# Optimization experiments

Hardware: AMD Instinct MI355X
Metric: run time of the kernel (lower is better)

The kernel has to match this reference:

```python
import jax, jax.numpy as jnp
import numpy as np

B, L, HID = 1, 2048, 4096
H, KV, D = 32, 2, 128
ROT = int(D * 0.5)  # partial rotary dims per head
THETA = 10000.0
SCALE = D ** -0.5


def _rope_tables(L, rot, theta):
    inv_freq = 1.0 / (theta ** (np.arange(0, rot, 2, dtype=np.float32) / rot))  # [rot/2]
    t = np.arange(L, dtype=np.float32)
    freqs = np.outer(t, inv_freq)  # [L, rot/2]
    return jnp.asarray(np.cos(freqs)), jnp.asarray(np.sin(freqs))


def setup_inputs() -> dict:
    key = jax.random.key(0)
    ks = jax.random.split(key, 8)
    s = HID ** -0.5
    x = jax.random.normal(ks[0], (B, L, HID), dtype=jnp.float32)
    Wq = jax.random.normal(ks[1], (HID, H * D), dtype=jnp.float32) * s
    Wk = jax.random.normal(ks[2], (HID, KV * D), dtype=jnp.float32) * s
    Wv = jax.random.normal(ks[3], (HID, KV * D), dtype=jnp.float32) * s
    Wo = jax.random.normal(ks[4], (H * D, HID), dtype=jnp.float32) * s
    bq = jax.random.normal(ks[5], (H * D,), dtype=jnp.float32) * 0.01
    bk = jax.random.normal(ks[6], (KV * D,), dtype=jnp.float32) * 0.01
    bv = jax.random.normal(ks[7], (KV * D,), dtype=jnp.float32) * 0.01
    cos, sin = _rope_tables(L, ROT, THETA)
    # additive causal mask
    causal = jnp.tril(jnp.ones((L, L), dtype=bool))
    attention_mask = jnp.where(causal, 0.0, -1e9)[None, None].astype(jnp.float32)
    return {"x": x, "Wq": Wq, "bq": bq, "Wk": Wk, "bk": bk, "Wv": Wv, "bv": bv,
            "Wo": Wo, "cos": cos, "sin": sin, "attention_mask": attention_mask}


def _apply_rope(t, cos, sin):
    # t: [B, h, L, D]; rotary on first ROT dims, pass-through on the rest
    t_rot, t_pass = t[..., :ROT], t[..., ROT:]
    x1, x2 = t_rot[..., : ROT // 2], t_rot[..., ROT // 2:]
    c = cos[None, None]  # [1,1,L,ROT/2]
    s = sin[None, None]
    rot = jnp.concatenate([x1 * c - x2 * s, x2 * c + x1 * s], axis=-1)
    return jnp.concatenate([rot, t_pass], axis=-1)


def reference(x, Wq, bq, Wk, bk, Wv, bv, Wo, cos, sin, attention_mask):
    Bx, Lx, _ = x.shape
    q = (x @ Wq + bq).reshape(Bx, Lx, H, D).transpose(0, 2, 1, 3)   # [B,H,L,D]
    k = (x @ Wk + bk).reshape(Bx, Lx, KV, D).transpose(0, 2, 1, 3)  # [B,KV,L,D]
    v = (x @ Wv + bv).reshape(Bx, Lx, KV, D).transpose(0, 2, 1, 3)
    q = _apply_rope(q, cos, sin)
    k = _apply_rope(k, cos, sin)
    # GQA: repeat KV heads
    rep = H // KV
    k = jnp.repeat(k, rep, axis=1)  # [B,H,L,D]
    v = jnp.repeat(v, rep, axis=1)
    w = jnp.einsum('bhqd,bhkd->bhqk', q, k) * SCALE + attention_mask
    w = jax.nn.softmax(w, axis=-1)
    o = jnp.einsum('bhqk,bhkd->bhqd', w, v)
    o = o.transpose(0, 2, 1, 3).reshape(Bx, Lx, H * D)
    return o @ Wo
```

## Files before the change

kernel.cpp:

```cpp
#include <hip/hip_runtime.h>
#include <stdint.h>

#define L_SEQ 2048
#define HID   4096
#define NH    32
#define NKV   2
#define DH    128
#define NQKV  4608
#define QSCALE 0.088388347648318447f

typedef __bf16 bf16x8 __attribute__((ext_vector_type(8)));
typedef float  f32x4  __attribute__((ext_vector_type(4)));

__device__ __forceinline__ unsigned short f2bf(float f) {
  union { float f; unsigned u; } cv; cv.f = f;
  unsigned u = cv.u;
  return (unsigned short)((u + 0x7fffu + ((u >> 16) & 1u)) >> 16);
}
__device__ __forceinline__ float bf2f(unsigned short h) {
  union { unsigned u; float f; } cv; cv.u = (unsigned)h << 16; return cv.f;
}

#define GLL16(gsrc, ldst)                                                              \
  __builtin_amdgcn_global_load_lds(                                                    \
      (const __attribute__((address_space(1))) unsigned int*)(gsrc),                   \
      (__attribute__((address_space(3))) unsigned int*)(ldst), 16, 0, 0)

__global__ __launch_bounds__(256) void cast_bf16_kernel(const float* __restrict__ in,
                                                        unsigned short* __restrict__ out,
                                                        int n4) {
  int i = blockIdx.x * 256 + threadIdx.x;
  if (i >= n4) return;
  float4 v = reinterpret_cast<const float4*>(in)[i];
  ushort4 o;
  o.x = f2bf(v.x); o.y = f2bf(v.y); o.z = f2bf(v.z); o.w = f2bf(v.w);
  reinterpret_cast<ushort4*>(out)[i] = o;
}

__global__ __launch_bounds__(256) void transpose_cast_kernel(const float* __restrict__ in,
                                                             unsigned short* __restrict__ out,
                                                             int R, int C) {
  __shared__ float tile[64][65];
  const int c0 = blockIdx.x * 64, r0 = blockIdx.y * 64;
  const int tid = threadIdx.x;
  #pragma unroll
  for (int it = 0; it < 4; ++it) {
    int row = it * 16 + (tid >> 4);
    float4 v = *reinterpret_cast<const float4*>(&in[(size_t)(r0 + row) * C + c0 + (tid & 15) * 4]);
    tile[row][(tid & 15) * 4 + 0] = v.x;
    tile[row][(tid & 15) * 4 + 1] = v.y;
    tile[row][(tid & 15) * 4 + 2] = v.z;
    tile[row][(tid & 15) * 4 + 3] = v.w;
  }
  __syncthreads();
  #pragma unroll
  for (int it = 0; it < 8; ++it) {
    int c  = it * 8 + (tid >> 5);
    int rp = tid & 31;
    unsigned u = (unsigned)f2bf(tile[2 * rp][c]) | ((unsigned)f2bf(tile[2 * rp + 1][c]) << 16);
    *reinterpret_cast<unsigned*>(&out[(size_t)(c0 + c) * R + r0 + 2 * rp]) = u;
  }
}

__global__ __launch_bounds__(256) void vtrans_kernel(const unsigned short* __restrict__ in,
                                                     unsigned short* __restrict__ out) {
  __shared__ unsigned short tile[64][72];
  const int l0 = blockIdx.x * 64, d0 = blockIdx.y * 64, g = blockIdx.z;
  const int tid = threadIdx.x;
  #pragma unroll
  for (int it = 0; it < 2; ++it) {
    int l = it * 32 + (tid >> 3);
    *reinterpret_cast<uint4*>(&tile[l][(tid & 7) * 8]) =
        *reinterpret_cast<const uint4*>(&in[((size_t)g * L_SEQ + l0 + l) * DH + d0 + (tid & 7) * 8]);
  }
  __syncthreads();
  #pragma unroll
  for (int it = 0; it < 2; ++it) {
    int d = it * 32 + (tid >> 3);
    unsigned short tmp[8];
    #pragma unroll
    for (int e = 0; e < 8; ++e) tmp[e] = tile[(tid & 7) * 8 + e][d];
    *reinterpret_cast<uint4*>(&out[((size_t)g * DH + d0 + d) * L_SEQ + l0 + (tid & 7) * 8]) =
        *reinterpret_cast<uint4*>(tmp);
  }
}

#define TBM 128
#define TBN 128
#define TBK 64

template <int MODE>
__global__ __launch_bounds__(256, 2) void gemm128_kernel(const unsigned short* __restrict__ A,
                                                         const unsigned short* __restrict__ Bt,
                                                         float* __restrict__ C,
                                                         const float* __restrict__ bq,
                                                         const float* __restrict__ bk,
                                                         const float* __restrict__ bv,
                                                         const float* __restrict__ cosT,
                                                         const float* __restrict__ sinT,
                                                         unsigned short* __restrict__ qb,
                                                         unsigned short* __restrict__ kb,
                                                         unsigned short* __restrict__ vlin,
                                                         int M, int N, int K) {
  __shared__ __attribute__((aligned(16))) unsigned short As[2][TBM * TBK];
  __shared__ __attribute__((aligned(16))) unsigned short Bs[2][TBN * TBK];
  const int tid = threadIdx.x;
  const int wave = tid >> 6, lane = tid & 63;
  const int lg = lane >> 4, ll = lane & 15;
  const int wm = wave >> 1, wn = wave & 1;

  int gx = gridDim.x, nwg = gx * gridDim.y;
  int flat = blockIdx.y * gx + blockIdx.x;
  int bx = blockIdx.x, by = blockIdx.y;
  if ((nwg & 7) == 0) {
    int t = (flat & 7) * (nwg >> 3) + (flat >> 3);
    bx = t % gx; by = t / gx;
  }
  const int m0 = by * TBM, n0 = bx * TBN;

  f32x4 acc[4][4] = {};
  const int NT = K >> 6;

  auto stage = [&](int t, int buf) {
    const int k0 = t * TBK;
    #pragma unroll
    for (int i = 0; i < 4; ++i) {
      int ci  = (i * 4 + wave) * 64 + lane;
      int row = ci >> 3;
      int cg  = (ci & 7) ^ (row & 7);
      GLL16(A + (size_t)(m0 + row) * K + k0 + cg * 8, &As[buf][(i * 4 + wave) * 512]);
    }
    #pragma unroll
    for (int i = 0; i < 4; ++i) {
      int ci  = (i * 4 + wave) * 64 + lane;
      int row = ci >> 3;
      int cg  = (ci & 7) ^ (row & 7);
      GLL16(Bt + (size_t)(n0 + row) * K + k0 + cg * 8, &Bs[buf][(i * 4 + wave) * 512]);
    }
  };

  stage(0, 0);
  stage(1, 1);

  for (int t = 0; t < NT; ++t) {
    const int cur = t & 1;
    if (t + 1 < NT) asm volatile("s_waitcnt vmcnt(8)" ::: "memory");
    else            asm volatile("s_waitcnt vmcnt(0)" ::: "memory");
    __builtin_amdgcn_s_barrier();

    const unsigned short* Ac = &As[cur][0];
    const unsigned short* Bc = &Bs[cur][0];
    bf16x8 afr[2][4], bfr[2][4];
    #pragma unroll
    for (int kk = 0; kk < 2; ++kk)
      #pragma unroll
      for (int i = 0; i < 4; ++i) {
        int ra = wm * 64 + i * 16 + ll;
        afr[kk][i] = *reinterpret_cast<const bf16x8*>(
            &Ac[ra * 64 + (((kk * 4 + lg) ^ (ra & 7)) * 8)]);
        int rb = wn * 64 + i * 16 + ll;
        bfr[kk][i] = *reinterpret_cast<const bf16x8*>(
            &Bc[rb * 64 + (((kk * 4 + lg) ^ (rb & 7)) * 8)]);
      }
    asm volatile("s_waitcnt lgkmcnt(0)" ::: "memory");
    __builtin_amdgcn_s_barrier();
    if (t + 2 < NT) stage(t + 2, cur);

    __builtin_amdgcn_s_setprio(1);
    #pragma unroll
    for (int kk = 0; kk < 2; ++kk)
      #pragma unroll
      for (int i = 0; i < 4; ++i)
        #pragma unroll
        for (int j = 0; j < 4; ++j)
          acc[i][j] = __builtin_amdgcn_mfma_f32_16x16x32_bf16(afr[kk][i], bfr[kk][j],
                                                              acc[i][j], 0, 0, 0);
    __builtin_amdgcn_s_setprio(0);
  }

  if (MODE == 0) {
    #pragma unroll
    for (int i = 0; i < 4; ++i)
      #pragma unroll
      for (int j = 0; j < 4; ++j) {
        int col  = n0 + wn * 64 + j * 16 + ll;
        int rowb = m0 + wm * 64 + i * 16 + lg * 4;
        #pragma unroll
        for (int r = 0; r < 4; ++r)
          C[(size_t)(rowb + r) * N + col] = acc[i][j][r];
      }
  } else {
    const int region = (n0 < 4096) ? 0 : ((n0 < 4352) ? 1 : 2);
    const int hh = (region == 0) ? (n0 >> 7) : ((region == 1) ? ((n0 - 4096) >> 7) : ((n0 - 4352) >> 7));
    const float* bias = (region == 0) ? bq : ((region == 1) ? bk : bv);
    #pragma unroll
    for (int j = 0; j < 4; ++j) {
      float bj = bias[hh * DH + wn * 64 + j * 16 + ll];
      #pragma unroll
      for (int i = 0; i < 4; ++i)
        #pragma unroll
        for (int r = 0; r < 4; ++r) acc[i][j][r] += bj;
    }
    if (region < 2 && wn == 0) {
      #pragma unroll
      for (int i = 0; i < 4; ++i)
        #pragma unroll
        for (int r = 0; r < 4; ++r) {
          int l = m0 + wm * 64 + i * 16 + lg * 4 + r;
          float c0 = cosT[l * 32 + ll],      s0 = sinT[l * 32 + ll];
          float c1 = cosT[l * 32 + 16 + ll], s1 = sinT[l * 32 + 16 + ll];
          float x10 = acc[i][0][r], x20 = acc[i][2][r];
          float x11 = acc[i][1][r], x21 = acc[i][3][r];
          acc[i][0][r] = x10 * c0 - x20 * s0;
          acc[i][2][r] = x20 * c0 + x10 * s0;
          acc[i][1][r] = x11 * c1 - x21 * s1;
          acc[i][3][r] = x21 * c1 + x11 * s1;
        }
    }
    const float scale = (region == 0) ? QSCALE : 1.f;
    unsigned short* dst = (region == 0) ? qb : ((region == 1) ? kb : vlin);
    #pragma unroll
    for (int i = 0; i < 4; ++i)
      #pragma unroll
      for (int j = 0; j < 4; ++j) {
        int d = wn * 64 + j * 16 + ll;
        #pragma unroll
        for (int r = 0; r < 4; ++r) {
          int l = m0 + wm * 64 + i * 16 + lg * 4 + r;
          dst[((size_t)hh * L_SEQ + l) * DH + d] = f2bf(acc[i][j][r] * scale);
        }
      }
  }
}

__global__ __launch_bounds__(256) void attn_kernel(const unsigned short* __restrict__ qg,
                                                   const unsigned short* __restrict__ kb,
                                                   const unsigned short* __restrict__ vt,
                                                   unsigned short* __restrict__ ob) {
  __shared__ __attribute__((aligned(16))) unsigned short Ks[2][64 * 128];
  __shared__ __attribute__((aligned(16))) unsigned short Vs[2][128 * 64];
  __shared__ __attribute__((aligned(16))) unsigned short Ps[4][16 * 64];

  const int pair = blockIdx.x, h = blockIdx.y;
  const int g = h >> 4;
  const int tid = threadIdx.x, wave = tid >> 6, lane = tid & 63;
  const int lg = lane >> 4, ll = lane & 15;

  const int krow = (lane >> 4);
  const int kcg0 = (lane & 15);
  const int vrow = (lane >> 3);
  const int vcg0 = (lane & 7);

  #pragma unroll
  for (int seg = 0; seg < 2; ++seg) {
    const int qt = seg ? (31 - pair) : pair;
    const int q0 = qt * 64 + wave * 16;

    bf16x8 qf[4];
    #pragma unroll
    for (int f = 0; f < 4; ++f)
      qf[f] = *reinterpret_cast<const bf16x8*>(
          qg + ((size_t)h * L_SEQ + q0 + ll) * DH + f * 32 + lg * 8);

    f32x4 of[8] = {};
    float m = -1e30f, lsum = 0.f;

    const int kvN = qt + 1;
    int cur = 0;

    #pragma unroll
    for (int c = 0; c < 4; ++c) {
      int issue = wave * 4 + c;
      int rk = issue * 4 + krow;
      GLL16(kb + ((size_t)g * L_SEQ + rk) * DH + (kcg0 ^ (rk & 7)) * 8, &Ks[0][issue * 512]);
      int rv = issue * 8 + vrow;
      GLL16(vt + ((size_t)g * DH + rv) * L_SEQ + (vcg0 ^ (rv & 7)) * 8, &Vs[0][issue * 512]);
    }
    __syncthreads();

    for (int t = 0; t < kvN; ++t) {
      if (t + 1 < kvN) {
        int kv1 = (t + 1) * 64;
        #pragma unroll
        for (int c = 0; c < 4; ++c) {
          int issue = wave * 4 + c;
          int rk = issue * 4 + krow;
          GLL16(kb + ((size_t)g * L_SEQ + kv1 + rk) * DH + (kcg0 ^ (rk & 7)) * 8,
                &Ks[cur ^ 1][issue * 512]);
          int rv = issue * 8 + vrow;
          GLL16(vt + ((size_t)g * DH + rv) * L_SEQ + kv1 + (vcg0 ^ (rv & 7)) * 8,
                &Vs[cur ^ 1][issue * 512]);
        }
      }

      f32x4 s[4] = {};
      const unsigned short* Kc = &Ks[cur][0];
      #pragma unroll
      for (int cf = 0; cf < 4; ++cf) {
        bf16x8 kf[4];
        #pragma unroll
        for (int f = 0; f < 4; ++f) {
          int rk = cf * 16 + ll;
          int cc = (f * 4 + lg) ^ (rk & 7);
          kf[f] = *reinterpret_cast<const bf16x8*>(&Kc[rk * 128 + cc * 8]);
        }
        __builtin_amdgcn_s_setprio(1);
        #pragma unroll
        for (int f = 0; f < 4; ++f)
          s[cf] = __builtin_amdgcn_mfma_f32_16x16x32_bf16(kf[f], qf[f], s[cf], 0, 0, 0);
        __builtin_amdgcn_s_setprio(0);
      }

      if (t == qt) {
        #pragma unroll
        for (int cf = 0; cf < 4; ++cf)
          #pragma unroll
          for (int r = 0; r < 4; ++r)
            if (cf * 16 + lg * 4 + r > wave * 16 + ll) s[cf][r] = -1e30f;
      }

      float pmax = -1e30f;
      #pragma unroll
      for (int cf = 0; cf < 4; ++cf)
        #pragma unroll
        for (int r = 0; r < 4; ++r) pmax = fmaxf(pmax, s[cf][r]);
      if (!__all(pmax - m <= 8.f)) {
        float mx = fmaxf(pmax, __shfl_xor(pmax, 16));
        mx = fmaxf(mx, __shfl_xor(mx, 32));
        float mnew = fmaxf(m, mx);
        float alpha = __expf(m - mnew);
        m = mnew;
        lsum *= alpha;
        float af[4];
        #pragma unroll
        for (int r = 0; r < 4; ++r) af[r] = __shfl(alpha, lg * 4 + r);
        #pragma unroll
        for (int ds = 0; ds < 8; ++ds)
          #pragma unroll
          for (int r = 0; r < 4; ++r) of[ds][r] *= af[r];
      }

      unsigned short* pw = &Ps[wave][0];
      float psum = 0.f;
      #pragma unroll
      for (int cf = 0; cf < 4; ++cf) {
        float p0 = __expf(s[cf][0] - m), p1 = __expf(s[cf][1] - m);
        float p2 = __expf(s[cf][2] - m), p3 = __expf(s[cf][3] - m);
        psum += (p0 + p1) + (p2 + p3);
        uint2 w;
        w.x = (unsigned)f2bf(p0) | ((unsigned)f2bf(p1) << 16);
        w.y = (unsigned)f2bf(p2) | ((unsigned)f2bf(p3) << 16);
        int chunk = (cf * 2 + (lg >> 1)) ^ (ll & 7);
        *reinterpret_cast<uint2*>(&pw[ll * 64 + chunk * 8 + (lg & 1) * 4]) = w;
      }
      lsum += psum;

      bf16x8 pa[2];
      #pragma unroll
      for (int ks = 0; ks < 2; ++ks)
        pa[ks] = *reinterpret_cast<const bf16x8*>(
            &pw[ll * 64 + (((ks * 4 + lg) ^ (ll & 7)) * 8)]);

      const unsigned short* Vc = &Vs[cur][0];
      #pragma unroll
      for (int ds = 0; ds < 8; ++ds) {
        bf16x8 vf[2];
        #pragma unroll
        for (int ks = 0; ks < 2; ++ks) {
          int dl = ds * 16 + ll;
          int cc = (ks * 4 + lg) ^ (dl & 7);
          vf[ks] = *reinterpret_cast<const bf16x8*>(&Vc[dl * 64 + cc * 8]);
        }
        __builtin_amdgcn_s_setprio(1);
        #pragma unroll
        for (int ks = 0; ks < 2; ++ks)
          of[ds] = __builtin_amdgcn_mfma_f32_16x16x32_bf16(pa[ks], vf[ks], of[ds], 0, 0, 0);
        __builtin_amdgcn_s_setprio(0);
      }

      __syncthreads();
      cur ^= 1;
    }

    float tot = lsum + __shfl_xor(lsum, 16);
    tot += __shfl_xor(tot, 32);
    float inv = 1.f / tot;
    float invr[4];
    #pragma unroll
    for (int r = 0; r < 4; ++r) invr[r] = __shfl(inv, lg * 4 + r);
    #pragma unroll
    for (int ds = 0; ds < 8; ++ds)
      #pragma unroll
      for (int r = 0; r < 4; ++r) {
        int row = q0 + lg * 4 + r;
        ob[(size_t)row * (NH * DH) + h * DH + ds * 16 + ll] = f2bf(of[ds][r] * invr[r]);
      }
    __syncthreads();
  }
}

extern "C" void kernel_launch(void* const* d_in, const int* in_sizes, int n_in,
                              void* d_out, int out_size, void* d_ws, size_t ws_size,
                              hipStream_t stream) {
  (void)in_sizes; (void)n_in; (void)out_size; (void)ws_size;
  const float* x    = (const float*)d_in[0];
  const float* Wq   = (const float*)d_in[1];
  const float* bq   = (const float*)d_in[2];
  const float* Wk   = (const float*)d_in[3];
  const float* bk   = (const float*)d_in[4];
  const float* Wv   = (const float*)d_in[5];
  const float* bv   = (const float*)d_in[6];
  const float* Wo   = (const float*)d_in[7];
  const float* cosT = (const float*)d_in[8];
  const float* sinT = (const float*)d_in[9];

  char* ws = (char*)d_ws;
  size_t off = 0;
  auto alloc = [&](size_t bytes) { void* p = ws + off; off += (bytes + 255) & ~(size_t)255; return p; };
  unsigned short* xb    = (unsigned short*)alloc((size_t)L_SEQ * HID * 2);
  unsigned short* Wqkvt = (unsigned short*)alloc((size_t)NQKV * HID * 2);
  unsigned short* Wot   = (unsigned short*)alloc((size_t)HID * HID * 2);
  unsigned short* qbuf  = (unsigned short*)alloc((size_t)NH * L_SEQ * DH * 2);
  unsigned short* kbuf  = (unsigned short*)alloc((size_t)NKV * L_SEQ * DH * 2);
  unsigned short* vlin  = (unsigned short*)alloc((size_t)NKV * L_SEQ * DH * 2);
  unsigned short* vtb   = (unsigned short*)alloc((size_t)NKV * DH * L_SEQ * 2);
  unsigned short* attno = (unsigned short*)alloc((size_t)L_SEQ * HID * 2);

  cast_bf16_kernel<<<(L_SEQ * HID / 4 + 255) / 256, 256, 0, stream>>>(x, xb, L_SEQ * HID / 4);
  transpose_cast_kernel<<<dim3(HID / 64, HID / 64), 256, 0, stream>>>(Wq, Wqkvt, HID, HID);
  transpose_cast_kernel<<<dim3(256 / 64, HID / 64), 256, 0, stream>>>(Wk, Wqkvt + (size_t)4096 * HID, HID, 256);
  transpose_cast_kernel<<<dim3(256 / 64, HID / 64), 256, 0, stream>>>(Wv, Wqkvt + (size_t)4352 * HID, HID, 256);
  transpose_cast_kernel<<<dim3(HID / 64, HID / 64), 256, 0, stream>>>(Wo, Wot, HID, HID);

  gemm128_kernel<1><<<dim3(NQKV / TBN, L_SEQ / TBM), 256, 0, stream>>>(
      xb, Wqkvt, nullptr, bq, bk, bv, cosT, sinT, qbuf, kbuf, vlin, L_SEQ, NQKV, HID);

  vtrans_kernel<<<dim3(L_SEQ / 64, DH / 64, NKV), 256, 0, stream>>>(vlin, vtb);

  attn_kernel<<<dim3(16, NH), 256, 0, stream>>>(qbuf, kbuf, vtb, attno);

  gemm128_kernel<0><<<dim3(HID / TBN, L_SEQ / TBM), 256, 0, stream>>>(
      attno, Wot, (float*)d_out, nullptr, nullptr, nullptr, nullptr, nullptr,
      nullptr, nullptr, nullptr, L_SEQ, HID, HID);
}
```

Measured before the change: 310.6 us.

## Deepen GEMM pipeline to four BK=32 stages; shuffle P fragments in attention

The GEMM mainloop moves from a double-buffered K-tile of 64 to a four-buffer ring of K=32 tiles with a 3-deep prefetch. The second barrier per iteration is removed and the next stage is issued right after the wait, so memory loads overlap MFMA work. The attention kernel drops the LDS round-trip for the softmax P matrix and rebuilds MFMA A-fragments with cross-lane shuffles, and it gets a launch bound requesting 2 blocks per CU. Risks include a WAR hazard on the ring buffer being reused without a second barrier, more shuffle instructions, and register pressure under the new occupancy bound.

```diff
diff --git a/kernel.cpp b/kernel.cpp
--- a/kernel.cpp
+++ b/kernel.cpp
@@ -19,6 +19,9 @@
 }
 __device__ __forceinline__ float bf2f(unsigned short h) {
   union { unsigned u; float f; } cv; cv.u = (unsigned)h << 16; return cv.f;
+}
+__device__ __forceinline__ unsigned pk2(float a, float b) {
+  return (unsigned)f2bf(a) | ((unsigned)f2bf(b) << 16);
 }
 
 #define GLL16(gsrc, ldst)                                                              \
@@ -87,7 +90,6 @@
 
 #define TBM 128
 #define TBN 128
-#define TBK 64
 
 template <int MODE>
 __global__ __launch_bounds__(256, 2) void gemm128_kernel(const unsigned short* __restrict__ A,
@@ -102,8 +104,8 @@
                                                          unsigned short* __restrict__ kb,
                                                          unsigned short* __restrict__ vlin,
                                                          int M, int N, int K) {
-  __shared__ __attribute__((aligned(16))) unsigned short As[2][TBM * TBK];
-  __shared__ __attribute__((aligned(16))) unsigned short Bs[2][TBN * TBK];
+  __shared__ __attribute__((aligned(16))) unsigned short As[4][TBM * 32];
+  __shared__ __attribute__((aligned(16))) unsigned short Bs[4][TBN * 32];
   const int tid = threadIdx.x;
   const int wave = tid >> 6, lane = tid & 63;
   const int lg = lane >> 4, ll = lane & 15;
@@ -119,62 +121,58 @@
   const int m0 = by * TBM, n0 = bx * TBN;
 
   f32x4 acc[4][4] = {};
-  const int NT = K >> 6;
+  const int NT = K >> 5;
 
   auto stage = [&](int t, int buf) {
-    const int k0 = t * TBK;
-    #pragma unroll
-    for (int i = 0; i < 4; ++i) {
+    const int k0 = t * 32;
+    #pragma unroll
+    for (int i = 0; i < 2; ++i) {
       int ci  = (i * 4 + wave) * 64 + lane;
-      int row = ci >> 3;
-      int cg  = (ci & 7) ^ (row & 7);
+      int row = ci >> 2;
+      int cg  = (ci & 3) ^ ((row >> 1) & 3);
       GLL16(A + (size_t)(m0 + row) * K + k0 + cg * 8, &As[buf][(i * 4 + wave) * 512]);
     }
     #pragma unroll
-    for (int i = 0; i < 4; ++i) {
+    for (int i = 0; i < 2; ++i) {
       int ci  = (i * 4 + wave) * 64 + lane;
-      int row = ci >> 3;
-      int cg  = (ci & 7) ^ (row & 7);
+      int row = ci >> 2;
+      int cg  = (ci & 3) ^ ((row >> 1) & 3);
       GLL16(Bt + (size_t)(n0 + row) * K + k0 + cg * 8, &Bs[buf][(i * 4 + wave) * 512]);
     }
   };
 
   stage(0, 0);
   stage(1, 1);
+  stage(2, 2);
 
   for (int t = 0; t < NT; ++t) {
-    const int cur = t & 1;
-    if (t + 1 < NT) asm volatile("s_waitcnt vmcnt(8)" ::: "memory");
-    else            asm volatile("s_waitcnt vmcnt(0)" ::: "memory");
+    const int cur = t & 3;
+    if (t + 2 < NT)      asm volatile("s_waitcnt vmcnt(8)" ::: "memory");
+    else if (t + 1 < NT) asm volatile("s_waitcnt vmcnt(4)" ::: "memory");
+    else                 asm volatile("s_waitcnt vmcnt(0)" ::: "memory");
     __builtin_amdgcn_s_barrier();
+    asm volatile("" ::: "memory");
+
+    if (t + 3 < NT) stage(t + 3, (t + 3) & 3);
 
     const unsigned short* Ac = &As[cur][0];
     const unsigned short* Bc = &Bs[cur][0];
-    bf16x8 afr[2][4], bfr[2][4];
-    #pragma unroll
-    for (int kk = 0; kk < 2; ++kk)
-      #pragma unroll
-      for (int i = 0; i < 4; ++i) {
-        int ra = wm * 64 + i * 16 + ll;
-        afr[kk][i] = *reinterpret_cast<const bf16x8*>(
-            &Ac[ra * 64 + (((kk * 4 + lg) ^ (ra & 7)) * 8)]);
-        int rb = wn * 64 + i * 16 + ll;
-        bfr[kk][i] = *reinterpret_cast<const bf16x8*>(
-            &Bc[rb * 64 + (((kk * 4 + lg) ^ (rb & 7)) * 8)]);
-      }
-    asm volatile("s_waitcnt lgkmcnt(0)" ::: "memory");
-    __builtin_amdgcn_s_barrier();
-    if (t + 2 < NT) stage(t + 2, cur);
-
+    bf16x8 afr[4], bfr[4];
+    #pragma unroll
+    for (int i = 0; i < 4; ++i) {
+      int ra = wm * 64 + i * 16 + ll;
+      afr[i] = *reinterpret_cast<const bf16x8*>(
+          &Ac[ra * 32 + ((lg ^ ((ra >> 1) & 3)) * 8)]);
+      int rb = wn * 64 + i * 16 + ll;
+      bfr[i] = *reinterpret_cast<const bf16x8*>(
+          &Bc[rb * 32 + ((lg ^ ((rb >> 1) & 3)) * 8)]);
+    }
     __builtin_amdgcn_s_setprio(1);
     #pragma unroll
-    for (int kk = 0; kk < 2; ++kk)
-      #pragma unroll
-      for (int i = 0; i < 4; ++i)
-        #pragma unroll
-        for (int j = 0; j < 4; ++j)
-          acc[i][j] = __builtin_amdgcn_mfma_f32_16x16x32_bf16(afr[kk][i], bfr[kk][j],
-                                                              acc[i][j], 0, 0, 0);
+    for (int i = 0; i < 4; ++i)
+      #pragma unroll
+      for (int j = 0; j < 4; ++j)
+        acc[i][j] = __builtin_amdgcn_mfma_f32_16x16x32_bf16(afr[i], bfr[j], acc[i][j], 0, 0, 0);
     __builtin_amdgcn_s_setprio(0);
   }
 
@@ -233,13 +231,12 @@
   }
 }
 
-__global__ __launch_bounds__(256) void attn_kernel(const unsigned short* __restrict__ qg,
-                                                   const unsigned short* __restrict__ kb,
-                                                   const unsigned short* __restrict__ vt,
-                                                   unsigned short* __restrict__ ob) {
+__global__ __launch_bounds__(256, 2) void attn_kernel(const unsigned short* __restrict__ qg,
+                                                      const unsigned short* __restrict__ kb,
+                                                      const unsigned short* __restrict__ vt,
+                                                      unsigned short* __restrict__ ob) {
   __shared__ __attribute__((aligned(16))) unsigned short Ks[2][64 * 128];
   __shared__ __attribute__((aligned(16))) unsigned short Vs[2][128 * 64];
-  __shared__ __attribute__((aligned(16))) unsigned short Ps[4][16 * 64];
 
   const int pair = blockIdx.x, h = blockIdx.y;
   const int g = h >> 4;
@@ -340,26 +337,41 @@
           for (int r = 0; r < 4; ++r) of[ds][r] *= af[r];
       }
 
-      unsigned short* pw = &Ps[wave][0];
+      unsigned wlo[4], whi[4];
       float psum = 0.f;
       #pragma unroll
       for (int cf = 0; cf < 4; ++cf) {
         float p0 = __expf(s[cf][0] - m), p1 = __expf(s[cf][1] - m);
         float p2 = __expf(s[cf][2] - m), p3 = __expf(s[cf][3] - m);
         psum += (p0 + p1) + (p2 + p3);
-        uint2 w;
-        w.x = (unsigned)f2bf(p0) | ((unsigned)f2bf(p1) << 16);
-        w.y = (unsigned)f2bf(p2) | ((unsigned)f2bf(p3) << 16);
-        int chunk = (cf * 2 + (lg >> 1)) ^ (ll & 7);
-        *reinterpret_cast<uint2*>(&pw[ll * 64 + chunk * 8 + (lg & 1) * 4]) = w;
+        wlo[cf] = pk2(p0, p1);
+        whi[cf] = pk2(p2, p3);
       }
       lsum += psum;
 
       bf16x8 pa[2];
-      #pragma unroll
-      for (int ks = 0; ks < 2; ++ks)
-        pa[ks] = *reinterpret_cast<const bf16x8*>(
-            &pw[ll * 64 + (((ks * 4 + lg) ^ (ll & 7)) * 8)]);
+      {
+        const int src0 = ((lg & 1) << 5) + ll;
+        const int src1 = src0 + 16;
+        const bool hi = (lg & 2) != 0;
+        #pragma unroll
+        for (int ks = 0; ks < 2; ++ks) {
+          int e0a = __shfl((int)wlo[ks * 2], src0);
+          int e1a = __shfl((int)whi[ks * 2], src0);
+          int e2a = __shfl((int)wlo[ks * 2], src1);
+          int e3a = __shfl((int)whi[ks * 2], src1);
+          int e0b = __shfl((int)wlo[ks * 2 + 1], src0);
+          int e1b = __shfl((int)whi[ks * 2 + 1], src0);
+          int e2b = __shfl((int)wlo[ks * 2 + 1], src1);
+          int e3b = __shfl((int)whi[ks * 2 + 1], src1);
+          union { int i[4]; bf16x8 v; } u;
+          u.i[0] = hi ? e0b : e0a;
+          u.i[1] = hi ? e1b : e1a;
+          u.i[2] = hi ? e2b : e2a;
+          u.i[3] = hi ? e3b : e3a;
+          pa[ks] = u.v;
+        }
+      }
 
       const unsigned short* Vc = &Vs[cur][0];
       #pragma unroll
```

Measured after the change: 381.2 us. 1.23x slower.
